# Optimization experiments

Hardware: AMD Instinct MI355X
Metric: run time of the kernel (lower is better)

Reference implementation:

```python
import jax, jax.numpy as jnp
import numpy as np
from jax import lax

# Model dims (match init_kwargs)
B, S, E, IMG = 4, 3, 7, 256
PH = 8            # patch size (2**size_ctimes)
H = IMG // PH     # 32, patch grid
D = 128           # patch_channels = mid_channels * patch_mult
NH, DK, DC = 4, 64, 128   # n_head, d_k, d_cond_in
DH = DC // NH     # per-head value dim
TEMB = 256
LK = 128          # kv length
GROUPS = 16       # GroupNorm32(16, D)
EPS = 1e-5


def conv2d(x, w, b, pad):
    y = lax.conv_general_dilated(x, w, (1, 1), [(pad, pad), (pad, pad)],
                                 dimension_numbers=('NCHW', 'OIHW', 'NCHW'))
    return y + b[None, :, None, None]


def setup_inputs() -> dict:
    key = jax.random.key(0)
    ks = jax.random.split(key, 16)
    def n(k, shape, s=1.0):
        return jax.random.normal(k, shape, jnp.float32) * s
    N = NH * B * H * H  # 16384
    return {
        'x': n(ks[0], (B, S, E, IMG, IMG)),
        'k_cond': n(ks[1], (N, LK, DK)),
        'v_cond': n(ks[2], (N, LK, DH)),
        'emb': n(ks[3], (B, TEMB)),
        'pos_embed': n(ks[4], (D, H, H), 0.02),
        'patch_w': n(ks[5], (D, E * PH * PH, 3, 3), 0.02),
        'patch_b': jnp.zeros((D,), jnp.float32),
        'gn_gamma': jnp.ones((D,), jnp.float32),
        'gn_beta': jnp.zeros((D,), jnp.float32),
        'fc1q_w': n(ks[6], (NH * DK, D), 0.05),
        'fc1q_b': jnp.zeros((NH * DK,), jnp.float32),
        'fc2q_w': n(ks[7], (S,), 0.3),
        'fc2q_b': jnp.zeros((), jnp.float32),
        'outproj_w': n(ks[8], (D, DC), 0.02),
        'outproj_b': jnp.zeros((D,), jnp.float32),
        'unpatch_w': n(ks[9], (E * PH * PH, D, 3, 3), 0.02),
        'unpatch_b': jnp.zeros((E * PH * PH,), jnp.float32),
        'mod_w': n(ks[10], (2 * E, TEMB), 0.02),
        'mod_b': jnp.zeros((2 * E,), jnp.float32),
        'enlarge_w': n(ks[11], (2 * E, E), 0.1),
        'enlarge_b': jnp.zeros((2 * E,), jnp.float32),
        'ff2_w': n(ks[12], (E, E), 0.1),
        'ff2_b': jnp.zeros((E,), jnp.float32),
    }


def reference(x, k_cond, v_cond, emb, pos_embed, patch_w, patch_b, gn_gamma,
              gn_beta, fc1q_w, fc1q_b, fc2q_w, fc2q_b, outproj_w, outproj_b,
              unpatch_w, unpatch_b, mod_w, mod_b, enlarge_w, enlarge_b,
              ff2_w, ff2_b):
    # ---- Patchize: (h nh)(w nw) -> (nh nw e) h w, then 3x3 conv + pos emb
    xp = x.reshape(B, S, E, H, PH, H, PH).transpose(0, 1, 4, 6, 2, 3, 5)
    xp = xp.reshape(B * S, PH * PH * E, H, H)
    xp = conv2d(xp, patch_w, patch_b, 1) + pos_embed[None]   # [B*S, D, H, H]
    xp = xp.reshape(B, S, D, H, H)

    # ---- Temporal_CrossAttention (note: torch .view = raw reshape, not transpose)
    xg = xp.reshape(B, D, S, H * H)                           # raw view
    g = xg.reshape(B, GROUPS, D // GROUPS, S, H * H)
    mu = g.mean(axis=(2, 3, 4), keepdims=True)
    var = g.var(axis=(2, 3, 4), keepdims=True)
    xn = ((g - mu) / jnp.sqrt(var + EPS)).reshape(B, D, S, H * H)
    xn = xn * gn_gamma[None, :, None, None] + gn_beta[None, :, None, None]

    Nq = B * H * H
    q_in = xn.reshape(Nq, D, S)                               # raw view
    q = jnp.einsum('od,nds->nos', fc1q_w, q_in) + fc1q_b[None, :, None]  # [Nq, NH*DK, S]
    q = jnp.einsum('nos,s->no', q, fc2q_w) + fc2q_b            # [Nq, NH*DK]
    qf = q.reshape(Nq * NH, DK)                                # head innermost

    scores = jnp.einsum('nd,nld->nl', qf, k_cond) * (1.0 / np.sqrt(DK))
    attn = jax.nn.softmax(scores, axis=-1)
    o = jnp.einsum('nl,nlc->nc', attn, v_cond)                 # [N, DH]
    # faithful raw view: N reinterpreted head-major
    o = o.reshape(NH, Nq, DH).transpose(1, 0, 2).reshape(Nq, DC)
    o = o.reshape(B, DC, H, H)                                 # raw view
    o = jnp.einsum('oc,bchw->bohw', outproj_w, o) + outproj_b[None, :, None, None]

    # ---- UnPatchize: 3x3 conv then (nh nw e) h w -> e (h nh)(w nw)
    u = conv2d(o, unpatch_w, unpatch_b, 1)                     # [B, E*PH*PH, H, H]
    u = u.reshape(B, PH, PH, E, H, H).transpose(0, 3, 4, 1, 5, 2)
    u = u.reshape(B, E, IMG, IMG)
    skip = u

    # ---- AdaptLayerNorm (LayerNorm over [E, IMG, IMG], adaLN scale/shift)
    c = jax.nn.silu(emb) @ mod_w.T + mod_b                     # [B, 2E]
    sc = c[:, :E, None, None]
    sh = c[:, E:, None, None]
    mu2 = u.mean(axis=(1, 2, 3), keepdims=True)
    var2 = u.var(axis=(1, 2, 3), keepdims=True)
    un = (u - mu2) / jnp.sqrt(var2 + EPS)
    un = un * (1.0 + sc) + sh

    # ---- FF: OgGateGeLU then 1x1 conv
    en = jnp.einsum('oc,bchw->bohw', enlarge_w, un) + enlarge_b[None, :, None, None]
    x1, x2 = en[:, :E], en[:, E:]
    gated = x1 * jax.nn.gelu(x2, approximate=False)
    hf = jax.nn.gelu(un, approximate=False) + gated
    ffo = jnp.einsum('oc,bchw->bohw', ff2_w, hf) + ff2_b[None, :, None, None]
    return ffo + skip
```

## Files before the change

kernel.cpp:

```cpp
#include <hip/hip_runtime.h>
#include <math.h>


__global__ void k_patchify(const float* __restrict__ x, float* __restrict__ xp_pad) {
    int idx = blockIdx.x * 256 + threadIdx.x;
    const int total = 12 * 448 * 34 * 34;
    if (idx >= total) return;
    int yx = idx % (34 * 34);
    int c  = (idx / (34 * 34)) % 448;
    int bs = idx / (448 * 34 * 34);
    int y = yx / 34, xc = yx % 34;
    float v = 0.0f;
    if (y >= 1 && y <= 32 && xc >= 1 && xc <= 32) {
        int h1 = y - 1, h2 = xc - 1;
        int p1 = c / 56, p2 = (c / 7) % 8, e = c % 7;
        v = x[(size_t)(bs * 7 + e) * 65536 + (size_t)(h1 * 8 + p1) * 256 + (h2 * 8 + p2)];
    }
    xp_pad[idx] = v;
}

__global__ void k_repack(const float* __restrict__ patch_w, const float* __restrict__ unpatch_w,
                         const float* __restrict__ fc1q_w,
                         float* __restrict__ pw9, float* __restrict__ uw9, float* __restrict__ qwT) {
    int idx = blockIdx.x * 256 + threadIdx.x;
    if (idx < 516096) {
        int d = idx % 128; int c = (idx / 128) % 448; int tap = idx / (128 * 448);
        pw9[idx] = patch_w[((size_t)d * 448 + c) * 9 + tap];
        int oc = idx % 448; int ic = (idx / 448) % 128; int tap2 = idx / (448 * 128);
        uw9[idx] = unpatch_w[((size_t)oc * 128 + ic) * 9 + tap2];
    }
    if (idx < 32768) {
        int o = idx % 256, dq = idx / 256;
        qwT[idx] = fc1q_w[o * 128 + dq];
    }
}

__global__ void k_init_xp2(const float* __restrict__ patch_b, const float* __restrict__ pos,
                           float* __restrict__ xp2) {
    int idx = blockIdx.x * 256 + threadIdx.x;
    int hw = idx & 1023; int d = (idx >> 10) & 127;
    xp2[idx] = patch_b[d] + pos[d * 1024 + hw];
}

__global__ __launch_bounds__(256) void k_conv1(const float* __restrict__ xp_pad,
                                               const float* __restrict__ pw9,
                                               float* __restrict__ xp2) {
    int htile = blockIdx.x, bs = blockIdx.y, tg = blockIdx.z;
    int h0 = htile * 4;
    int tid = threadIdx.x;
    int sp0 = (tid & 15) * 8;
    int d0  = (tid >> 4) * 8;
    __shared__ __align__(16) float As[8][4][36];
    __shared__ __align__(16) float Ws[8][128];
    float acc[8][8];
#pragma unroll
    for (int i = 0; i < 8; ++i)
#pragma unroll
        for (int j = 0; j < 8; ++j) acc[i][j] = 0.0f;

    const float* inb = xp_pad + (size_t)bs * 448 * 1156;
    for (int tap = tg * 3; tap < tg * 3 + 3; ++tap) {
        int kh = tap / 3, kw = tap % 3;
        for (int c0 = 0; c0 < 448; c0 += 8) {
#pragma unroll
            for (int t = 0; t < 4; ++t) {
                int j = tid + t * 256;
                int k = j >> 7, sp = j & 127;
                int r = sp >> 5, wv = sp & 31;
                As[k][r][wv] = inb[(size_t)(c0 + k) * 1156 + (h0 + r + kh) * 34 + (wv + kw)];
            }
            const float* wb = pw9 + ((size_t)tap * 448 + c0) * 128;
#pragma unroll
            for (int t = 0; t < 4; ++t) {
                int j = tid + t * 256;
                Ws[j >> 7][j & 127] = wb[j];
            }
            __syncthreads();
            int r = sp0 >> 5, cc = sp0 & 31;
#pragma unroll
            for (int k = 0; k < 8; ++k) {
                float4 a0 = *(const float4*)&As[k][r][cc];
                float4 a1 = *(const float4*)&As[k][r][cc + 4];
                float4 w0 = *(const float4*)&Ws[k][d0];
                float4 w1 = *(const float4*)&Ws[k][d0 + 4];
                float av[8] = {a0.x, a0.y, a0.z, a0.w, a1.x, a1.y, a1.z, a1.w};
                float wv[8] = {w0.x, w0.y, w0.z, w0.w, w1.x, w1.y, w1.z, w1.w};
#pragma unroll
                for (int i = 0; i < 8; ++i)
#pragma unroll
                    for (int j = 0; j < 8; ++j) acc[i][j] += av[i] * wv[j];
            }
            __syncthreads();
        }
    }
    size_t base = (size_t)bs * 131072 + (size_t)h0 * 32;
#pragma unroll
    for (int j = 0; j < 8; ++j)
#pragma unroll
        for (int i = 0; i < 8; ++i)
            atomicAdd(&xp2[base + (size_t)(d0 + j) * 1024 + sp0 + i], acc[i][j]);
}

__global__ void k_gstats(const float* __restrict__ xp2, float* __restrict__ gstat) {
    int bg = blockIdx.x;
    const float* p = xp2 + (size_t)bg * 24576;
    float s = 0.0f, s2 = 0.0f;
    for (int i = threadIdx.x; i < 24576; i += 256) { float v = p[i]; s += v; s2 += v * v; }
#pragma unroll
    for (int off = 32; off; off >>= 1) { s += __shfl_down(s, off); s2 += __shfl_down(s2, off); }
    __shared__ float ws[4], ws2[4];
    int w = threadIdx.x >> 6, lane = threadIdx.x & 63;
    if (lane == 0) { ws[w] = s; ws2[w] = s2; }
    __syncthreads();
    if (threadIdx.x == 0) {
        float S = ws[0] + ws[1] + ws[2] + ws[3];
        float S2 = ws2[0] + ws2[1] + ws2[2] + ws2[3];
        float mu = S * (1.0f / 24576.0f);
        float var = S2 * (1.0f / 24576.0f) - mu * mu;
        gstat[bg * 2] = mu;
        gstat[bg * 2 + 1] = rsqrtf(var + 1e-5f);
    }
}

__global__ void k_qred(const float* __restrict__ xp2, const float* __restrict__ gstat,
                       const float* __restrict__ gamma, const float* __restrict__ beta,
                       const float* __restrict__ w2, float* __restrict__ qred) {
    int idx = blockIdx.x * 256 + threadIdx.x;
    int dq = idx & 127, n = idx >> 7;
    int b = n >> 10;
    int f = (n & 1023) * 384 + dq * 3;
    const float* src = xp2 + (size_t)b * 393216 + f;
    float out = 0.0f;
#pragma unroll
    for (int s = 0; s < 3; ++s) {
        int ff = f + s;
        int g = ff / 24576;
        int gi = ff / 3072;
        float mu = gstat[(b * 16 + g) * 2], rstd = gstat[(b * 16 + g) * 2 + 1];
        float v = (src[s] - mu) * rstd * gamma[gi] + beta[gi];
        out += w2[s] * v;
    }
    qred[idx] = out;
}

__global__ void k_qgemm(const float* __restrict__ qred, const float* __restrict__ qwT,
                        const float* __restrict__ fc1q_b, const float* __restrict__ w2,
                        const float* __restrict__ fc2q_b, float* __restrict__ q) {
    int o = threadIdx.x;
    int n0 = blockIdx.x * 4;
    __shared__ float sq[4][128];
    for (int t = threadIdx.x; t < 512; t += 256) sq[t >> 7][t & 127] = qred[n0 * 128 + t];
    __syncthreads();
    float a0 = 0, a1 = 0, a2 = 0, a3 = 0;
    for (int k = 0; k < 128; ++k) {
        float wv = qwT[k * 256 + o];
        a0 += wv * sq[0][k]; a1 += wv * sq[1][k]; a2 += wv * sq[2][k]; a3 += wv * sq[3][k];
    }
    float bias = fc1q_b[o] * (w2[0] + w2[1] + w2[2]) + fc2q_b[0];
    q[(size_t)(n0 + 0) * 256 + o] = a0 + bias;
    q[(size_t)(n0 + 1) * 256 + o] = a1 + bias;
    q[(size_t)(n0 + 2) * 256 + o] = a2 + bias;
    q[(size_t)(n0 + 3) * 256 + o] = a3 + bias;
}

__global__ __launch_bounds__(256) void k_attn(const float* __restrict__ q,
                                              const float* __restrict__ kc,
                                              const float* __restrict__ vc,
                                              float* __restrict__ o2) {
    int w = threadIdx.x >> 6, lane = threadIdx.x & 63;
    int r = blockIdx.x * 4 + w;
    int n = r >> 2, nh = r & 3;
    __shared__ float sQ[4][64];
    __shared__ float sP[4][128];
    sQ[w][lane] = q[(size_t)n * 256 + nh * 64 + lane];
    __syncthreads();
    const float4* K4 = (const float4*)(kc + (size_t)r * 8192);
    const float4* q4 = (const float4*)sQ[w];
    float s0 = 0.0f, s1 = 0.0f;
#pragma unroll
    for (int i = 0; i < 16; ++i) {
        float4 qv = q4[i];
        float4 k0 = K4[lane * 16 + i];
        float4 k1 = K4[(64 + lane) * 16 + i];
        s0 += qv.x * k0.x + qv.y * k0.y + qv.z * k0.z + qv.w * k0.w;
        s1 += qv.x * k1.x + qv.y * k1.y + qv.z * k1.z + qv.w * k1.w;
    }
    s0 *= 0.125f; s1 *= 0.125f;
    float mx = fmaxf(s0, s1);
#pragma unroll
    for (int off = 32; off; off >>= 1) mx = fmaxf(mx, __shfl_xor(mx, off));
    float p0 = __expf(s0 - mx), p1 = __expf(s1 - mx);
    float sum = p0 + p1;
#pragma unroll
    for (int off = 32; off; off >>= 1) sum += __shfl_xor(sum, off);
    float inv = 1.0f / sum;
    sP[w][lane] = p0 * inv;
    sP[w][64 + lane] = p1 * inv;
    __syncthreads();
    const float* V = vc + (size_t)r * 4096;
    int c = lane & 31, half = lane >> 5;
    float acc = 0.0f;
#pragma unroll 8
    for (int l = 0; l < 64; ++l) {
        int ll = half * 64 + l;
        acc += sP[w][ll] * V[ll * 32 + c];
    }
    acc += __shfl_down(acc, 32);
    if (lane < 32) {
        int m = r & 4095, a = r >> 12;
        o2[(size_t)m * 128 + a * 32 + lane] = acc;
    }
}

__global__ void k_outproj(const float* __restrict__ o2, const float* __restrict__ opw,
                          const float* __restrict__ opb, float* __restrict__ op_pad) {
    int hw = blockIdx.x * 256 + threadIdx.x;
    int o = blockIdx.y, b = blockIdx.z;
    const float* src = o2 + (size_t)b * 131072 + hw;
    const float* wrow = opw + o * 128;
    float acc = opb[o];
#pragma unroll 4
    for (int cc = 0; cc < 128; ++cc) acc += wrow[cc] * src[(size_t)cc * 1024];
    int h = hw >> 5, wv = hw & 31;
    op_pad[((size_t)(b * 128 + o) * 34 + 1 + h) * 34 + 1 + wv] = acc;
}

__global__ __launch_bounds__(256) void k_conv2(const float* __restrict__ op_pad,
                                               const float* __restrict__ uw9,
                                               const float* __restrict__ upb,
                                               float* __restrict__ u) {
    int htile = blockIdx.x, b = blockIdx.y, nt = blockIdx.z;
    int h0 = htile * 4;
    int tid = threadIdx.x;
    int sp0 = (tid & 15) * 8;
    int d0 = (tid >> 4) * 4;
    __shared__ __align__(16) float As[8][4][36];
    __shared__ __align__(16) float Ws[8][64];
    float acc[8][4];
#pragma unroll
    for (int j = 0; j < 4; ++j) {
        float bias = upb[nt * 64 + d0 + j];
#pragma unroll
        for (int i = 0; i < 8; ++i) acc[i][j] = bias;
    }
    const float* inb = op_pad + (size_t)b * 128 * 1156;
    for (int tap = 0; tap < 9; ++tap) {
        int kh = tap / 3, kw = tap % 3;
        for (int c0 = 0; c0 < 128; c0 += 8) {
#pragma unroll
            for (int t = 0; t < 4; ++t) {
                int j = tid + t * 256;
                int k = j >> 7, sp = j & 127;
                int rr = sp >> 5, wv = sp & 31;
                As[k][rr][wv] = inb[(size_t)(c0 + k) * 1156 + (h0 + rr + kh) * 34 + (wv + kw)];
            }
#pragma unroll
            for (int t = 0; t < 2; ++t) {
                int jj = tid + t * 256;
                int k = jj >> 6, oc = jj & 63;
                Ws[k][oc] = uw9[((size_t)tap * 128 + c0 + k) * 448 + nt * 64 + oc];
            }
            __syncthreads();
            int rr = sp0 >> 5, cc = sp0 & 31;
#pragma unroll
            for (int k = 0; k < 8; ++k) {
                float4 a0 = *(const float4*)&As[k][rr][cc];
                float4 a1 = *(const float4*)&As[k][rr][cc + 4];
                float4 w0 = *(const float4*)&Ws[k][d0];
                float av[8] = {a0.x, a0.y, a0.z, a0.w, a1.x, a1.y, a1.z, a1.w};
                float wv4[4] = {w0.x, w0.y, w0.z, w0.w};
#pragma unroll
                for (int i = 0; i < 8; ++i)
#pragma unroll
                    for (int j = 0; j < 4; ++j) acc[i][j] += av[i] * wv4[j];
            }
            __syncthreads();
        }
    }
#pragma unroll
    for (int j = 0; j < 4; ++j) {
        int oc = nt * 64 + d0 + j;
        int e = oc % 7, p2 = (oc / 7) & 7, p1 = oc / 56;
#pragma unroll
        for (int i = 0; i < 8; ++i) {
            int sp = sp0 + i;
            int hh = h0 + (sp >> 5), ww = sp & 31;
            u[((size_t)(b * 7 + e) * 256 + hh * 8 + p1) * 256 + ww * 8 + p2] = acc[i][j];
        }
    }
}

__global__ void k_lnpart(const float* __restrict__ u, float* __restrict__ acc2) {
    int b = blockIdx.x >> 6, blk = blockIdx.x & 63;
    const float* p = u + (size_t)b * 458752 + (size_t)blk * 7168;
    float s = 0.0f, s2 = 0.0f;
    for (int i = threadIdx.x; i < 7168; i += 256) { float v = p[i]; s += v; s2 += v * v; }
#pragma unroll
    for (int off = 32; off; off >>= 1) { s += __shfl_down(s, off); s2 += __shfl_down(s2, off); }
    __shared__ float ws[4], ws2[4];
    int w = threadIdx.x >> 6, lane = threadIdx.x & 63;
    if (lane == 0) { ws[w] = s; ws2[w] = s2; }
    __syncthreads();
    if (threadIdx.x == 0) {
        atomicAdd(&acc2[b * 2], ws[0] + ws[1] + ws[2] + ws[3]);
        atomicAdd(&acc2[b * 2 + 1], ws2[0] + ws2[1] + ws2[2] + ws2[3]);
    }
}

__global__ void k_finalize(const float* __restrict__ acc2, const float* __restrict__ emb,
                           const float* __restrict__ mod_w, const float* __restrict__ mod_b,
                           float* __restrict__ mstat) {
    int b = blockIdx.x;
    __shared__ float se[256];
    float ev = emb[b * 256 + threadIdx.x];
    se[threadIdx.x] = ev / (1.0f + __expf(-ev));
    __syncthreads();
    if (threadIdx.x < 14) {
        float a = mod_b[threadIdx.x];
        const float* wr = mod_w + threadIdx.x * 256;
        for (int t = 0; t < 256; ++t) a += wr[t] * se[t];
        mstat[b * 16 + threadIdx.x] = a;
    } else if (threadIdx.x == 14) {
        mstat[b * 16 + 14] = acc2[b * 2] * (1.0f / 458752.0f);
    } else if (threadIdx.x == 15) {
        float mu = acc2[b * 2] * (1.0f / 458752.0f);
        float var = acc2[b * 2 + 1] * (1.0f / 458752.0f) - mu * mu;
        mstat[b * 16 + 15] = rsqrtf(var + 1e-5f);
    }
}

__global__ void k_final(const float* __restrict__ u, const float* __restrict__ mstat,
                        const float* __restrict__ ew, const float* __restrict__ eb,
                        const float* __restrict__ f2w, const float* __restrict__ f2b,
                        float* __restrict__ out) {
    int pix = blockIdx.x * 256 + threadIdx.x;
    int b = pix >> 16, p = pix & 65535;
    const float* ub = u + (size_t)b * 458752 + p;
    float mu = mstat[b * 16 + 14], rstd = mstat[b * 16 + 15];
    float un[7], skip[7];
#pragma unroll
    for (int e = 0; e < 7; ++e) {
        float v = ub[(size_t)e * 65536];
        skip[e] = v;
        float nv = (v - mu) * rstd;
        un[e] = nv * (1.0f + mstat[b * 16 + e]) + mstat[b * 16 + 7 + e];
    }
    float hf[7];
#pragma unroll
    for (int e = 0; e < 7; ++e) {
        float x1 = eb[e], x2 = eb[7 + e];
#pragma unroll
        for (int cc = 0; cc < 7; ++cc) {
            x1 += ew[e * 7 + cc] * un[cc];
            x2 += ew[(7 + e) * 7 + cc] * un[cc];
        }
        float g2 = 0.5f * x2 * (1.0f + erff(x2 * 0.70710678118f));
        float gu = 0.5f * un[e] * (1.0f + erff(un[e] * 0.70710678118f));
        hf[e] = gu + x1 * g2;
    }
#pragma unroll
    for (int o = 0; o < 7; ++o) {
        float a = f2b[o];
#pragma unroll
        for (int cc = 0; cc < 7; ++cc) a += f2w[o * 7 + cc] * hf[cc];
        out[(size_t)b * 458752 + (size_t)o * 65536 + p] = a + skip[o];
    }
}

extern "C" void kernel_launch(void* const* d_in, const int* in_sizes, int n_in,
                              void* d_out, int out_size, void* d_ws, size_t ws_size,
                              hipStream_t stream) {
    const float* x         = (const float*)d_in[0];
    const float* k_cond    = (const float*)d_in[1];
    const float* v_cond    = (const float*)d_in[2];
    const float* emb       = (const float*)d_in[3];
    const float* pos_embed = (const float*)d_in[4];
    const float* patch_w   = (const float*)d_in[5];
    const float* patch_b   = (const float*)d_in[6];
    const float* gn_gamma  = (const float*)d_in[7];
    const float* gn_beta   = (const float*)d_in[8];
    const float* fc1q_w    = (const float*)d_in[9];
    const float* fc1q_b    = (const float*)d_in[10];
    const float* fc2q_w    = (const float*)d_in[11];
    const float* fc2q_b    = (const float*)d_in[12];
    const float* outproj_w = (const float*)d_in[13];
    const float* outproj_b = (const float*)d_in[14];
    const float* unpatch_w = (const float*)d_in[15];
    const float* unpatch_b = (const float*)d_in[16];
    const float* mod_w     = (const float*)d_in[17];
    const float* mod_b     = (const float*)d_in[18];
    const float* enlarge_w = (const float*)d_in[19];
    const float* enlarge_b = (const float*)d_in[20];
    const float* ff2_w     = (const float*)d_in[21];
    const float* ff2_b     = (const float*)d_in[22];
    float* out = (float*)d_out;

    float* ws = (float*)d_ws;
    size_t off = 0;
    auto alloc = [&](size_t n) { float* p = ws + off; off += n; return p; };
    float* xp_pad = alloc(12ull * 448 * 1156);
    float* pw9    = alloc(516096);
    float* uw9    = alloc(516096);
    float* qwT    = alloc(32768);
    float* xp2    = alloc(1572864);
    float* gstat  = alloc(128);
    float* qred   = alloc(524288);
    float* qbuf   = alloc(1048576);
    float* o2     = alloc(524288);
    float* op_pad = alloc(4ull * 128 * 1156);
    float* ubuf   = alloc(1835008);
    float* acc2   = alloc(8);
    float* mstat  = alloc(64);

    hipMemsetAsync(acc2, 0, 8 * sizeof(float), stream);
    hipMemsetAsync(op_pad, 0, 4ull * 128 * 1156 * sizeof(float), stream);

    k_patchify<<<(12 * 448 * 1156 + 255) / 256, 256, 0, stream>>>(x, xp_pad);
    k_repack<<<2016, 256, 0, stream>>>(patch_w, unpatch_w, fc1q_w, pw9, uw9, qwT);
    k_init_xp2<<<6144, 256, 0, stream>>>(patch_b, pos_embed, xp2);
    k_conv1<<<dim3(8, 12, 3), 256, 0, stream>>>(xp_pad, pw9, xp2);
    k_gstats<<<64, 256, 0, stream>>>(xp2, gstat);
    k_qred<<<2048, 256, 0, stream>>>(xp2, gstat, gn_gamma, gn_beta, fc2q_w, qred);
    k_qgemm<<<1024, 256, 0, stream>>>(qred, qwT, fc1q_b, fc2q_w, fc2q_b, qbuf);
    k_attn<<<4096, 256, 0, stream>>>(qbuf, k_cond, v_cond, o2);
    k_outproj<<<dim3(4, 128, 4), 256, 0, stream>>>(o2, outproj_w, outproj_b, op_pad);
    k_conv2<<<dim3(8, 4, 7), 256, 0, stream>>>(op_pad, uw9, unpatch_b, ubuf);
    k_lnpart<<<256, 256, 0, stream>>>(ubuf, acc2);
    k_finalize<<<4, 256, 0, stream>>>(acc2, emb, mod_w, mod_b, mstat);
    k_final<<<1024, 256, 0, stream>>>(ubuf, mstat, enlarge_w, enlarge_b, ff2_w, ff2_b, out);
}
```

Baseline: 1.688 ms.

## Split conv1 over channel quarters with partial buffers instead of atomics; retile conv2

Conv1 now splits the reduction across four channel quarters instead of three tap groups. Each block writes its partial sums to its own buffer with plain float4 stores, and a new reduction kernel adds the partials plus bias and positional embedding, replacing the atomicAdd epilogue and the init kernel. Both convolutions use smaller spatial tiles of 2 rows and a 16-deep K step, which doubles the block count to fill more CUs. The partial buffer aliases later workspace, so the op_pad memset moves after the reduction. In exchange, per-thread register tiles shrink, which lowers arithmetic intensity, and the partials add extra memory traffic.

```diff
diff --git a/kernel.cpp b/kernel.cpp
--- a/kernel.cpp
+++ b/kernel.cpp
@@ -35,70 +35,71 @@
     }
 }
 
-__global__ void k_init_xp2(const float* __restrict__ patch_b, const float* __restrict__ pos,
-                           float* __restrict__ xp2) {
+__global__ __launch_bounds__(256) void k_conv1(const float* __restrict__ xp_pad,
+                                               const float* __restrict__ pw9,
+                                               float* __restrict__ part1) {
+    int stile = blockIdx.x, bs = blockIdx.y, cq = blockIdx.z;
+    int h0 = stile * 2;
+    int tid = threadIdx.x;
+    int sp0 = (tid & 15) * 4;
+    int d0  = (tid >> 4) * 8;
+    __shared__ __align__(16) float As[16][2][36];
+    __shared__ __align__(16) float Ws[16][128];
+    float acc[4][8];
+#pragma unroll
+    for (int i = 0; i < 4; ++i)
+#pragma unroll
+        for (int j = 0; j < 8; ++j) acc[i][j] = 0.0f;
+
+    const float* inb = xp_pad + (size_t)bs * 448 * 1156;
+    for (int tap = 0; tap < 9; ++tap) {
+        int kh = tap / 3, kw = tap % 3;
+        for (int c0 = cq * 112; c0 < cq * 112 + 112; c0 += 16) {
+#pragma unroll
+            for (int t = 0; t < 4; ++t) {
+                int j = tid + t * 256;
+                int k = j >> 6, sp = j & 63;
+                int r = sp >> 5, wv = sp & 31;
+                As[k][r][wv] = inb[(size_t)(c0 + k) * 1156 + (h0 + r + kh) * 34 + (wv + kw)];
+            }
+            const float* wb = pw9 + ((size_t)tap * 448 + c0) * 128;
+#pragma unroll
+            for (int t = 0; t < 8; ++t) {
+                int j = tid + t * 256;
+                Ws[j >> 7][j & 127] = wb[j];
+            }
+            __syncthreads();
+            int r = sp0 >> 5, cc = sp0 & 31;
+#pragma unroll
+            for (int k = 0; k < 16; ++k) {
+                float4 a  = *(const float4*)&As[k][r][cc];
+                float4 w0 = *(const float4*)&Ws[k][d0];
+                float4 w1 = *(const float4*)&Ws[k][d0 + 4];
+                float av[4] = {a.x, a.y, a.z, a.w};
+                float wv[8] = {w0.x, w0.y, w0.z, w0.w, w1.x, w1.y, w1.z, w1.w};
+#pragma unroll
+                for (int i = 0; i < 4; ++i)
+#pragma unroll
+                    for (int j = 0; j < 8; ++j) acc[i][j] += av[i] * wv[j];
+            }
+            __syncthreads();
+        }
+    }
+    float* dst = part1 + (size_t)(cq * 12 + bs) * 131072 + stile * 64;
+#pragma unroll
+    for (int j = 0; j < 8; ++j) {
+        float4 v = make_float4(acc[0][j], acc[1][j], acc[2][j], acc[3][j]);
+        *(float4*)&dst[(size_t)(d0 + j) * 1024 + sp0] = v;
+    }
+}
+
+__global__ void k_red1(const float* __restrict__ part1, const float* __restrict__ patch_b,
+                       const float* __restrict__ pos, float* __restrict__ xp2) {
     int idx = blockIdx.x * 256 + threadIdx.x;
     int hw = idx & 1023; int d = (idx >> 10) & 127;
-    xp2[idx] = patch_b[d] + pos[d * 1024 + hw];
-}
-
-__global__ __launch_bounds__(256) void k_conv1(const float* __restrict__ xp_pad,
-                                               const float* __restrict__ pw9,
-                                               float* __restrict__ xp2) {
-    int htile = blockIdx.x, bs = blockIdx.y, tg = blockIdx.z;
-    int h0 = htile * 4;
-    int tid = threadIdx.x;
-    int sp0 = (tid & 15) * 8;
-    int d0  = (tid >> 4) * 8;
-    __shared__ __align__(16) float As[8][4][36];
-    __shared__ __align__(16) float Ws[8][128];
-    float acc[8][8];
-#pragma unroll
-    for (int i = 0; i < 8; ++i)
-#pragma unroll
-        for (int j = 0; j < 8; ++j) acc[i][j] = 0.0f;
-
-    const float* inb = xp_pad + (size_t)bs * 448 * 1156;
-    for (int tap = tg * 3; tap < tg * 3 + 3; ++tap) {
-        int kh = tap / 3, kw = tap % 3;
-        for (int c0 = 0; c0 < 448; c0 += 8) {
-#pragma unroll
-            for (int t = 0; t < 4; ++t) {
-                int j = tid + t * 256;
-                int k = j >> 7, sp = j & 127;
-                int r = sp >> 5, wv = sp & 31;
-                As[k][r][wv] = inb[(size_t)(c0 + k) * 1156 + (h0 + r + kh) * 34 + (wv + kw)];
-            }
-            const float* wb = pw9 + ((size_t)tap * 448 + c0) * 128;
-#pragma unroll
-            for (int t = 0; t < 4; ++t) {
-                int j = tid + t * 256;
-                Ws[j >> 7][j & 127] = wb[j];
-            }
-            __syncthreads();
-            int r = sp0 >> 5, cc = sp0 & 31;
-#pragma unroll
-            for (int k = 0; k < 8; ++k) {
-                float4 a0 = *(const float4*)&As[k][r][cc];
-                float4 a1 = *(const float4*)&As[k][r][cc + 4];
-                float4 w0 = *(const float4*)&Ws[k][d0];
-                float4 w1 = *(const float4*)&Ws[k][d0 + 4];
-                float av[8] = {a0.x, a0.y, a0.z, a0.w, a1.x, a1.y, a1.z, a1.w};
-                float wv[8] = {w0.x, w0.y, w0.z, w0.w, w1.x, w1.y, w1.z, w1.w};
-#pragma unroll
-                for (int i = 0; i < 8; ++i)
-#pragma unroll
-                    for (int j = 0; j < 8; ++j) acc[i][j] += av[i] * wv[j];
-            }
-            __syncthreads();
-        }
-    }
-    size_t base = (size_t)bs * 131072 + (size_t)h0 * 32;
-#pragma unroll
-    for (int j = 0; j < 8; ++j)
-#pragma unroll
-        for (int i = 0; i < 8; ++i)
-            atomicAdd(&xp2[base + (size_t)(d0 + j) * 1024 + sp0 + i], acc[i][j]);
+    float v = patch_b[d] + pos[d * 1024 + hw];
+    v += part1[idx] + part1[idx + 1572864] + part1[idx + 2 * 1572864] + part1[idx + 3 * 1572864];
+    xp2[idx] = v;
 }
 
 __global__ void k_gstats(const float* __restrict__ xp2, float* __restrict__ gstat) {
@@ -229,48 +230,47 @@
                                                const float* __restrict__ uw9,
                                                const float* __restrict__ upb,
                                                float* __restrict__ u) {
-    int htile = blockIdx.x, b = blockIdx.y, nt = blockIdx.z;
-    int h0 = htile * 4;
+    int stile = blockIdx.x, b = blockIdx.y, nt = blockIdx.z;
+    int h0 = stile * 2;
     int tid = threadIdx.x;
-    int sp0 = (tid & 15) * 8;
-    int d0 = (tid >> 4) * 4;
-    __shared__ __align__(16) float As[8][4][36];
-    __shared__ __align__(16) float Ws[8][64];
-    float acc[8][4];
+    int sp0 = (tid & 15) * 4;
+    int oc0 = (tid >> 4) * 4;
+    __shared__ __align__(16) float As[16][2][36];
+    __shared__ __align__(16) float Ws[16][64];
+    float acc[4][4];
 #pragma unroll
     for (int j = 0; j < 4; ++j) {
-        float bias = upb[nt * 64 + d0 + j];
-#pragma unroll
-        for (int i = 0; i < 8; ++i) acc[i][j] = bias;
+        float bias = upb[nt * 64 + oc0 + j];
+#pragma unroll
+        for (int i = 0; i < 4; ++i) acc[i][j] = bias;
     }
     const float* inb = op_pad + (size_t)b * 128 * 1156;
     for (int tap = 0; tap < 9; ++tap) {
         int kh = tap / 3, kw = tap % 3;
-        for (int c0 = 0; c0 < 128; c0 += 8) {
+        for (int c0 = 0; c0 < 128; c0 += 16) {
 #pragma unroll
             for (int t = 0; t < 4; ++t) {
                 int j = tid + t * 256;
-                int k = j >> 7, sp = j & 127;
-                int rr = sp >> 5, wv = sp & 31;
-                As[k][rr][wv] = inb[(size_t)(c0 + k) * 1156 + (h0 + rr + kh) * 34 + (wv + kw)];
-            }
-#pragma unroll
-            for (int t = 0; t < 2; ++t) {
-                int jj = tid + t * 256;
-                int k = jj >> 6, oc = jj & 63;
+                int k = j >> 6, sp = j & 63;
+                int r = sp >> 5, wv = sp & 31;
+                As[k][r][wv] = inb[(size_t)(c0 + k) * 1156 + (h0 + r + kh) * 34 + (wv + kw)];
+            }
+#pragma unroll
+            for (int t = 0; t < 4; ++t) {
+                int j = tid + t * 256;
+                int k = j >> 6, oc = j & 63;
                 Ws[k][oc] = uw9[((size_t)tap * 128 + c0 + k) * 448 + nt * 64 + oc];
             }
             __syncthreads();
-            int rr = sp0 >> 5, cc = sp0 & 31;
-#pragma unroll
-            for (int k = 0; k < 8; ++k) {
-                float4 a0 = *(const float4*)&As[k][rr][cc];
-                float4 a1 = *(const float4*)&As[k][rr][cc + 4];
-                float4 w0 = *(const float4*)&Ws[k][d0];
-                float av[8] = {a0.x, a0.y, a0.z, a0.w, a1.x, a1.y, a1.z, a1.w};
-                float wv4[4] = {w0.x, w0.y, w0.z, w0.w};
-#pragma unroll
-                for (int i = 0; i < 8; ++i)
+            int r = sp0 >> 5, cc = sp0 & 31;
+#pragma unroll
+            for (int k = 0; k < 16; ++k) {
+                float4 a = *(const float4*)&As[k][r][cc];
+                float4 w = *(const float4*)&Ws[k][oc0];
+                float av[4] = {a.x, a.y, a.z, a.w};
+                float wv4[4] = {w.x, w.y, w.z, w.w};
+#pragma unroll
+                for (int i = 0; i < 4; ++i)
 #pragma unroll
                     for (int j = 0; j < 4; ++j) acc[i][j] += av[i] * wv4[j];
             }
@@ -279,10 +279,10 @@
     }
 #pragma unroll
     for (int j = 0; j < 4; ++j) {
-        int oc = nt * 64 + d0 + j;
+        int oc = nt * 64 + oc0 + j;
         int e = oc % 7, p2 = (oc / 7) & 7, p1 = oc / 56;
 #pragma unroll
-        for (int i = 0; i < 8; ++i) {
+        for (int i = 0; i < 4; ++i) {
             int sp = sp0 + i;
             int hh = h0 + (sp >> 5), ww = sp & 31;
             u[((size_t)(b * 7 + e) * 256 + hh * 8 + p1) * 256 + ww * 8 + p2] = acc[i][j];
@@ -404,27 +404,28 @@
     float* qwT    = alloc(32768);
     float* xp2    = alloc(1572864);
     float* gstat  = alloc(128);
-    float* qred   = alloc(524288);
-    float* qbuf   = alloc(1048576);
-    float* o2     = alloc(524288);
-    float* op_pad = alloc(4ull * 128 * 1156);
-    float* ubuf   = alloc(1835008);
     float* acc2   = alloc(8);
     float* mstat  = alloc(64);
+    float* part1  = ws + off;
+    float* qred   = part1;
+    float* qbuf   = qred + 524288;
+    float* o2     = qbuf + 1048576;
+    float* op_pad = o2 + 524288;
+    float* ubuf   = op_pad + 591872;
 
     hipMemsetAsync(acc2, 0, 8 * sizeof(float), stream);
-    hipMemsetAsync(op_pad, 0, 4ull * 128 * 1156 * sizeof(float), stream);
 
     k_patchify<<<(12 * 448 * 1156 + 255) / 256, 256, 0, stream>>>(x, xp_pad);
     k_repack<<<2016, 256, 0, stream>>>(patch_w, unpatch_w, fc1q_w, pw9, uw9, qwT);
-    k_init_xp2<<<6144, 256, 0, stream>>>(patch_b, pos_embed, xp2);
-    k_conv1<<<dim3(8, 12, 3), 256, 0, stream>>>(xp_pad, pw9, xp2);
+    k_conv1<<<dim3(16, 12, 4), 256, 0, stream>>>(xp_pad, pw9, part1);
+    k_red1<<<6144, 256, 0, stream>>>(part1, patch_b, pos_embed, xp2);
+    hipMemsetAsync(op_pad, 0, 4ull * 128 * 1156 * sizeof(float), stream);
     k_gstats<<<64, 256, 0, stream>>>(xp2, gstat);
     k_qred<<<2048, 256, 0, stream>>>(xp2, gstat, gn_gamma, gn_beta, fc2q_w, qred);
     k_qgemm<<<1024, 256, 0, stream>>>(qred, qwT, fc1q_b, fc2q_w, fc2q_b, qbuf);
     k_attn<<<4096, 256, 0, stream>>>(qbuf, k_cond, v_cond, o2);
     k_outproj<<<dim3(4, 128, 4), 256, 0, stream>>>(o2, outproj_w, outproj_b, op_pad);
-    k_conv2<<<dim3(8, 4, 7), 256, 0, stream>>>(op_pad, uw9, unpatch_b, ubuf);
+    k_conv2<<<dim3(16, 4, 7), 256, 0, stream>>>(op_pad, uw9, unpatch_b, ubuf);
     k_lnpart<<<256, 256, 0, stream>>>(ubuf, acc2);
     k_finalize<<<4, 256, 0, stream>>>(acc2, emb, mod_w, mod_b, mstat);
     k_final<<<1024, 256, 0, stream>>>(ubuf, mstat, enlarge_w, enlarge_b, ff2_w, ff2_b, out);
```

New measurement: 1.374 ms. 18.6% less time.
